# Kernel optimization log

Measured on AMD Instinct MI355X. Metric: run time of the kernel, lower is better.

## Reference

```python
import jax, jax.numpy as jnp
import numpy as np

IOU_HI = 0.5
IOU_LO = 0.0
ROI_BS = 256
POS_RATIO = 0.25
BG = 20  # background class id; valid classes 0..BG-1
NUM_POS = int(ROI_BS * POS_RATIO)
DELTAS_SCALING = np.array([10.0, 10.0, 5.0, 5.0], dtype=np.float32)  # (x, y, w, h)


def _make_boxes(key, shape):
    ka, kb = jax.random.split(key)
    c = jax.random.uniform(ka, shape + (2,), minval=0.05, maxval=0.95)
    s = jax.random.uniform(kb, shape + (2,), minval=0.02, maxval=0.4)
    lo = jnp.clip(c - s / 2, 0.0, 1.0)
    hi = jnp.clip(c + s / 2, 0.0, 1.0)
    return jnp.concatenate([lo, hi], -1)  # (y1, x1, y2, x2), normalized


def setup_inputs() -> dict:
    key = jax.random.key(0)
    k1, k2, k3 = jax.random.split(key, 3)
    B, N, G = 32, 12000, 200
    rois = _make_boxes(k1, (B, N))
    gt_boxes = _make_boxes(k2, (B, G))
    # class == BG marks a padded / invalid GT box
    gt_class_ids = jax.random.randint(k3, (B, G), 0, BG + 1).astype(jnp.int32)
    return {"rois": rois, "gt_class_ids": gt_class_ids, "gt_boxes": gt_boxes}


def _iou(rois, gts):
    # rois [N,4], gts [G,4] in (y1,x1,y2,x2) -> [N,G]
    y1 = jnp.maximum(rois[:, None, 0], gts[None, :, 0])
    x1 = jnp.maximum(rois[:, None, 1], gts[None, :, 1])
    y2 = jnp.minimum(rois[:, None, 2], gts[None, :, 2])
    x2 = jnp.minimum(rois[:, None, 3], gts[None, :, 3])
    inter = jnp.clip(y2 - y1, 0.0) * jnp.clip(x2 - x1, 0.0)
    ar = (rois[:, 2] - rois[:, 0]) * (rois[:, 3] - rois[:, 1])
    ag = (gts[:, 2] - gts[:, 0]) * (gts[:, 3] - gts[:, 1])
    return inter / (ar[:, None] + ag[None, :] - inter + 1e-8)


def _encode(r, g):
    # (tx, ty, tw, th) * scaling, r/g: [K,4] in (y1,x1,y2,x2)
    eps = 1e-6
    rh = r[:, 2] - r[:, 0]; rw = r[:, 3] - r[:, 1]
    rcy = r[:, 0] + rh / 2; rcx = r[:, 1] + rw / 2
    gh = g[:, 2] - g[:, 0]; gw = g[:, 3] - g[:, 1]
    gcy = g[:, 0] + gh / 2; gcx = g[:, 1] + gw / 2
    tx = (gcx - rcx) / (rw + eps)
    ty = (gcy - rcy) / (rh + eps)
    tw = jnp.log(jnp.maximum(gw, eps) / (rw + eps))
    th = jnp.log(jnp.maximum(gh, eps) / (rh + eps))
    return jnp.stack([tx, ty, tw, th], -1) * jnp.asarray(DELTAS_SCALING)


def _per_image(rois, gt_cls, gt_boxes):
    iou = _iou(rois, gt_boxes)                       # [N,G]
    valid_gt = gt_cls < BG
    iou = jnp.where(valid_gt[None, :], iou, -1.0)
    max_iou = iou.max(1)                             # [N]
    best_gt = iou.argmax(1)                          # [N]
    pos = max_iou >= IOU_HI
    neg = (max_iou < IOU_HI) & (max_iou >= IOU_LO)

    # deterministic sampling: highest-IoU positives / negatives first
    pos_val, pos_idx = jax.lax.top_k(jnp.where(pos, max_iou, -1.0), NUM_POS)
    pos_ok = pos_val > 0.0
    neg_val, neg_idx = jax.lax.top_k(jnp.where(neg, max_iou + 2.0, -1.0), ROI_BS)
    neg_ok = neg_val > 0.0

    rP = jnp.arange(NUM_POS, dtype=jnp.float32)
    rN = jnp.arange(ROI_BS, dtype=jnp.float32)
    prio = jnp.concatenate([jnp.where(pos_ok, 1e9 - rP, -1e9 - rP),
                            jnp.where(neg_ok, 1e6 - rN, -1e6 - rN)])
    cand_idx = jnp.concatenate([pos_idx, neg_idx])
    cand_pos = jnp.concatenate([pos_ok, jnp.zeros(ROI_BS, bool)])
    _, sel = jax.lax.top_k(prio, ROI_BS)
    sel_roi = cand_idx[sel]                          # [ROI_BS]
    sel_is_pos = cand_pos[sel]                       # [ROI_BS]

    labels = jnp.where(sel_is_pos, gt_cls[best_gt[sel_roi]], BG)
    rois_sel = rois[sel_roi]                         # [ROI_BS,4]
    gts_sel = gt_boxes[best_gt[sel_roi]]             # [ROI_BS,4]
    t = _encode(rois_sel, gts_sel) * sel_is_pos[:, None].astype(rois.dtype)

    cls_onehot = jax.nn.one_hot(labels, BG + 1, dtype=rois.dtype)   # [ROI_BS,BG+1]
    onehot_fg = jax.nn.one_hot(labels, BG, dtype=rois.dtype)        # zero row for bg
    mask4 = jnp.repeat(onehot_fg, 4, axis=1)                        # [ROI_BS,4*BG]
    deltas_full = (onehot_fg[:, :, None] * t[:, None, :]).reshape(ROI_BS, 4 * BG)
    reg = jnp.concatenate([mask4, deltas_full], -1)                 # [ROI_BS,8*BG]
    return rois_sel, cls_onehot, reg


def reference(rois, gt_class_ids, gt_boxes):
    return jax.vmap(_per_image)(rois, gt_class_ids, gt_boxes)
```

## Files before the change

### kernel.cpp

```cpp
#include <hip/hip_runtime.h>
#include <stdint.h>

#pragma clang fp contract(off)

#define BATCH 32
#define NROI  12000
#define NGT   200
#define BGCLS 20
#define ROIBS 256
#define NPOS  64
#define NBIN  1024
#define CAP   2048
#define TSEL  1024
#define VPT2  12
#define HSH   16
#define HST   (NBIN + 2)
#define DELTA 1e-6f

__device__ __forceinline__ void roi_maxiou_all(const float4* cbox, const float* carea,
                                               int nv, float ry1, float rx1,
                                               float ry2, float rx2,
                                               float& best, int& bj) {
#pragma clang fp contract(off)
  float ar = (ry2 - ry1) * (rx2 - rx1);
  best = -1.0f; bj = 0;
#pragma unroll 4
  for (int j = 0; j < nv; ++j) {
    float4 q = cbox[j];
    float yy1 = fmaxf(ry1, q.x);
    float xx1 = fmaxf(rx1, q.y);
    float yy2 = fminf(ry2, q.z);
    float xx2 = fminf(rx2, q.w);
    float inter = fmaxf(yy2 - yy1, 0.0f) * fmaxf(xx2 - xx1, 0.0f);
    float den = ((ar + carea[j]) - inter) + 1e-8f;
    float iou = inter / den;
    if (iou > best) { best = iou; bj = j; }
  }
}

__device__ __forceinline__ float approx_max(const float4* cbox, const float* carea,
                                            int nv, float4 r) {
  float ar = (r.z - r.x) * (r.w - r.y);
  float va = -1.0f, vb = -1.0f;
#pragma unroll 4
  for (int j = 0; j < nv; ++j) {
    float4 q = cbox[j];
    float yy1 = fmaxf(r.x, q.x);
    float xx1 = fmaxf(r.y, q.y);
    float yy2 = fminf(r.z, q.z);
    float xx2 = fminf(r.w, q.w);
    float inter = fmaxf(yy2 - yy1, 0.0f) * fmaxf(xx2 - xx1, 0.0f);
    float den = ((ar + carea[j]) - inter) + 1e-8f;
    float a = inter * __builtin_amdgcn_rcpf(den);
    if (j & 1) vb = fmaxf(vb, a); else va = fmaxf(va, a);
  }
  return fmaxf(va, vb);
}

__global__ __launch_bounds__(256) void k_ioumax(const float* __restrict__ rois,
                                                const int* __restrict__ gtc,
                                                const float* __restrict__ gtb,
                                                float* __restrict__ max_iou) {
  __shared__ float4 cbox[NGT];
  __shared__ float carea[NGT];
  __shared__ int snv, wtmp[4];
  const int b = blockIdx.y;
  const int tid = threadIdx.x;

  {
    bool valid = false; float4 p = make_float4(0.f, 0.f, 0.f, 0.f);
    if (tid < NGT) {
      p = *(const float4*)(gtb + ((size_t)b * NGT + tid) * 4);
      valid = gtc[(size_t)b * NGT + tid] < BGCLS;
    }
    unsigned long long m = __ballot(valid);
    int w = tid >> 6;
    if ((tid & 63) == 0) wtmp[w] = __popcll(m);
    __syncthreads();
    if (tid == 0) snv = wtmp[0] + wtmp[1] + wtmp[2] + wtmp[3];
    if (valid) {
      int off = 0;
      for (int i = 0; i < w; ++i) off += wtmp[i];
      int pos = off + __popcll(m & ((1ull << (tid & 63)) - 1ull));
      cbox[pos] = p;
      carea[pos] = (p.z - p.x) * (p.w - p.y);
    }
    __syncthreads();
  }
  int n = blockIdx.x * 256 + tid;
  if (n >= NROI) return;
  const float4 r = *(const float4*)(rois + ((size_t)b * NROI + n) * 4);
  max_iou[(size_t)b * NROI + n] = approx_max(cbox, carea, snv, r);
}

template <bool USE_WS>
__global__ __launch_bounds__(TSEL) void k_sel(const float* __restrict__ rois,
                                              const int* __restrict__ gtc,
                                              const float* __restrict__ gtb,
                                              const float* __restrict__ max_iou,
                                              float* __restrict__ out) {
#pragma clang fp contract(off)
  __shared__ float4 cbox[NGT];
  __shared__ float carea[NGT];
  __shared__ int ccls[NGT];
  __shared__ int snv, wtmp[16];
  __shared__ int wtot[16], wnext[16];
  __shared__ int plist[CAP];
  __shared__ unsigned long long keyl[CAP];
  __shared__ int bjl[CAP];
  __shared__ int hs[HSH][HST];
  __shared__ int ss[NBIN];
  __shared__ int sel_r[ROIBS];
  __shared__ int sel_b[ROIBS];
  __shared__ int scnt, sX, sT, sPos;
  const int b = blockIdx.x;
  const int tid = threadIdx.x;
  const int lane = tid & 63;

  {
    bool valid = false; float4 p = make_float4(0.f, 0.f, 0.f, 0.f); int cls = BGCLS;
    if (tid < NGT) {
      p = *(const float4*)(gtb + ((size_t)b * NGT + tid) * 4);
      cls = gtc[(size_t)b * NGT + tid];
      valid = (cls < BGCLS);
    }
    unsigned long long m = __ballot(valid);
    int w = tid >> 6;
    if ((tid & 63) == 0) wtmp[w] = __popcll(m);
    if (tid < ROIBS) { sel_r[tid] = 0; sel_b[tid] = 0; }
    __syncthreads();
    if (tid == 0) { int s = 0; for (int i = 0; i < 16; ++i) s += wtmp[i]; snv = s; }
    if (valid) {
      int off = 0;
      for (int i = 0; i < w; ++i) off += wtmp[i];
      int pos = off + __popcll(m & ((1ull << (tid & 63)) - 1ull));
      cbox[pos] = p;
      carea[pos] = (p.z - p.x) * (p.w - p.y);
      ccls[pos] = cls;
    }
    __syncthreads();
  }
  const int nv = snv;

  float v[VPT2];
#pragma unroll
  for (int i = 0; i < VPT2; ++i) {
    int n = tid + (i << 10);
    if (n < NROI) {
      if constexpr (USE_WS) {
        v[i] = max_iou[(size_t)b * NROI + n];
      } else {
        const float4 r = *(const float4*)(rois + ((size_t)b * NROI + n) * 4);
        v[i] = approx_max(cbox, carea, nv, r);
      }
    } else v[i] = -3.0f;
  }

  auto mkbin = [](unsigned kh, unsigned base, int shift) -> int {
    int bin = ((int)(kh - base)) >> shift;
    return max(min(bin, NBIN - 1), 0);
  };

  auto find_T = [&](int needv) -> int {
    if (tid == 0) sT = 0;
    __syncthreads();
    int cnt_bin = 0;
#pragma unroll
    for (int i = 0; i < HSH; ++i) cnt_bin += hs[i][tid];
    const int w = tid >> 6;
    int sfx = cnt_bin;
#pragma unroll
    for (int off = 1; off < 64; off <<= 1) {
      int t = __shfl_down(sfx, off, 64);
      sfx += (lane + off < 64) ? t : 0;
    }
    if (lane == 0) wtot[w] = sfx;
    __syncthreads();
    if (tid < 16) {
      int s = 0;
      for (int i = tid + 1; i < 16; ++i) s += wtot[i];
      wnext[tid] = s;
    }
    __syncthreads();
    const int suffix = sfx + wnext[w];
    ss[tid] = suffix;
    __syncthreads();
    int nxt = (tid + 1 < NBIN) ? ss[tid + 1] : 0;
    if (suffix >= needv && nxt < needv) sT = tid;
    __syncthreads();
    return sT;
  };

  auto rank_of = [&](unsigned long long ki, int cnt) -> int {
    int r0 = 0, r1 = 0, r2 = 0, r3 = 0;
    int j = 0;
    for (; j + 4 <= cnt; j += 4) {
      r0 += (keyl[j + 0] > ki);
      r1 += (keyl[j + 1] > ki);
      r2 += (keyl[j + 2] > ki);
      r3 += (keyl[j + 3] > ki);
    }
    for (; j < cnt; ++j) r0 += (keyl[j] > ki);
    return r0 + r1 + r2 + r3;
  };

  const int sh = tid & (HSH - 1);

  for (int i = tid; i < HSH * HST; i += TSEL) ((int*)hs)[i] = 0;
  if (tid == 0) { scnt = 0; sX = 0; sPos = 0; }
  __syncthreads();
#pragma unroll
  for (int i = 0; i < VPT2; ++i) {
    int n = tid + (i << 10);
    float x = v[i];
    bool inb = (n < NROI) && (x >= 0.5f - DELTA);
    if (inb) atomicAdd(&hs[sh][mkbin(__float_as_uint(x), 0x3F000000u, 13)], 1);
    bool bnd = inb && (x < 0.5f + DELTA);
    unsigned long long mx = __ballot(bnd);
    if (lane == 0 && mx) atomicAdd(&sX, __popcll(mx));
  }
  __syncthreads();
  const int XB = sX;
  const int Tp = max(find_T(NPOS + XB) - 2, 0);
#pragma unroll
  for (int i = 0; i < VPT2; ++i) {
    int n = tid + (i << 10);
    float x = v[i];
    bool pred = (n < NROI) && (x >= 0.5f - DELTA) &&
                (mkbin(__float_as_uint(x), 0x3F000000u, 13) >= Tp);
    unsigned long long mk = __ballot(pred);
    int c = __popcll(mk);
    int bs = 0;
    if (lane == 0 && c) bs = atomicAdd(&scnt, c);
    bs = __shfl(bs, 0, 64);
    if (pred) {
      int idx = bs + __popcll(mk & ((1ull << lane) - 1ull));
      if (idx < CAP) plist[idx] = n;
    }
  }
  __syncthreads();
  const int cntp = min(scnt, CAP);
  for (int i = tid; i < cntp; i += TSEL) {
    int n = plist[i];
    const float4 r = *(const float4*)(rois + ((size_t)b * NROI + n) * 4);
    float best; int bj;
    roi_maxiou_all(cbox, carea, nv, r.x, r.y, r.z, r.w, best, bj);
    bool ok = (best >= 0.5f);
    keyl[i] = ok ? (((unsigned long long)__float_as_uint(best) << 32)
                   | (unsigned)(0x7fffffff - n)) : 0ull;
    bjl[i] = bj;
    if (ok) atomicAdd(&sPos, 1);
  }
  __syncthreads();
  const int P = min(sPos, NPOS);
  for (int i = tid; i < cntp; i += TSEL) {
    unsigned long long ki = keyl[i];
    if (ki) {
      int rank = rank_of(ki, cntp);
      if (rank < P) {
        sel_r[rank] = 0x7fffffff - (int)(ki & 0xffffffffu);
        sel_b[rank] = bjl[i];
      }
    }
  }
  __syncthreads();

  const int need = ROIBS - P;
  for (int i = tid; i < HSH * HST; i += TSEL) ((int*)hs)[i] = 0;
  if (tid == 0) scnt = 0;
  __syncthreads();
#pragma unroll
  for (int i = 0; i < VPT2; ++i) {
    int n = tid + (i << 10);
    float x = v[i];
    if (n < NROI && x < 0.5f + DELTA)
      atomicAdd(&hs[sh][mkbin(__float_as_uint(x + 2.0f), 0x40000000u, 11)], 1);
  }
  __syncthreads();
  const int Tn = max(find_T(need + XB) - 2, 0);
#pragma unroll
  for (int i = 0; i < VPT2; ++i) {
    int n = tid + (i << 10);
    float x = v[i];
    bool pred = (n < NROI) && (x < 0.5f + DELTA) &&
                (mkbin(__float_as_uint(x + 2.0f), 0x40000000u, 11) >= Tn);
    unsigned long long mk = __ballot(pred);
    int c = __popcll(mk);
    int bs = 0;
    if (lane == 0 && c) bs = atomicAdd(&scnt, c);
    bs = __shfl(bs, 0, 64);
    if (pred) {
      int idx = bs + __popcll(mk & ((1ull << lane) - 1ull));
      if (idx < CAP) plist[idx] = n;
    }
  }
  __syncthreads();
  const int cntn = min(scnt, CAP);
  for (int i = tid; i < cntn; i += TSEL) {
    int n = plist[i];
    const float4 r = *(const float4*)(rois + ((size_t)b * NROI + n) * 4);
    float best; int bj;
    roi_maxiou_all(cbox, carea, nv, r.x, r.y, r.z, r.w, best, bj);
    bool ok = (best < 0.5f);
    keyl[i] = ok ? (((unsigned long long)__float_as_uint(best + 2.0f) << 32)
                   | (unsigned)(0x7fffffff - n)) : 0ull;
    bjl[i] = bj;
  }
  __syncthreads();
  for (int i = tid; i < cntn; i += TSEL) {
    unsigned long long ki = keyl[i];
    if (ki) {
      int rank = rank_of(ki, cntn);
      if (rank < need) {
        sel_r[P + rank] = 0x7fffffff - (int)(ki & 0xffffffffu);
        sel_b[P + rank] = bjl[i];
      }
    }
  }
  __syncthreads();

  {
    const int slot = tid >> 2, q = tid & 3;
    const int r = sel_r[slot];
    const int bj = sel_b[slot];
    const int isp = (slot < P) ? 1 : 0;
    const float4 rv = *(const float4*)(rois + ((size_t)b * NROI + r) * 4);
    float ry1 = rv.x, rx1 = rv.y, ry2 = rv.z, rx2 = rv.w;
    int label = isp ? ccls[bj] : BGCLS;

    float* out1 = out;
    float* out2 = out + (size_t)BATCH * ROIBS * 4;
    float* out3 = out + (size_t)BATCH * ROIBS * 25;
    size_t row = (size_t)b * ROIBS + slot;

    if (q == 0) {
      *(float4*)(out1 + row * 4) = rv;
      float* o2 = out2 + row * 21;
      for (int c = 0; c <= BGCLS; ++c) o2[c] = (c == label) ? 1.0f : 0.0f;
    }

    float t0 = 0.f, t1 = 0.f, t2 = 0.f, t3 = 0.f;
    if (isp) {
      const float eps = 1e-6f;
      float4 g = cbox[bj];
      float gy1 = g.x, gx1 = g.y, gy2 = g.z, gx2 = g.w;
      float rh = ry2 - ry1, rw = rx2 - rx1;
      float rcy = ry1 + rh * 0.5f, rcx = rx1 + rw * 0.5f;
      float gh = gy2 - gy1, gw = gx2 - gx1;
      float gcy = gy1 + gh * 0.5f, gcx = gx1 + gw * 0.5f;
      t0 = ((gcx - rcx) / (rw + eps)) * 10.0f;
      t1 = ((gcy - rcy) / (rh + eps)) * 10.0f;
      t2 = logf(fmaxf(gw, eps) / (rw + eps)) * 5.0f;
      t3 = logf(fmaxf(gh, eps) / (rh + eps)) * 5.0f;
    }
    int m0 = label * 4;
    float* o3 = out3 + row * 160;
    for (int c = q * 10; c < q * 10 + 10; ++c) {
      float4 wv = make_float4(0.f, 0.f, 0.f, 0.f);
      if (isp) {
        float* wp = &wv.x;
#pragma unroll
        for (int jj = 0; jj < 4; ++jj) {
          int e = c * 4 + jj;
          float x = 0.f;
          if (e >= m0 && e < m0 + 4) x = 1.0f;
          int d = e - 80 - m0;
          if (d == 0) x = t0; else if (d == 1) x = t1;
          else if (d == 2) x = t2; else if (d == 3) x = t3;
          wp[jj] = x;
        }
      }
      *(float4*)(o3 + c * 4) = wv;
    }
  }
}

extern "C" void kernel_launch(void* const* d_in, const int* in_sizes, int n_in,
                              void* d_out, int out_size, void* d_ws, size_t ws_size,
                              hipStream_t stream) {
  const float* rois = (const float*)d_in[0];
  const int*   gtc  = (const int*)d_in[1];
  const float* gtb  = (const float*)d_in[2];
  float*       out  = (float*)d_out;

  size_t need = (size_t)BATCH * NROI * sizeof(float);
  if (d_ws && ws_size >= need) {
    float* mi = (float*)d_ws;
    k_ioumax<<<dim3((NROI + 255) / 256, BATCH), 256, 0, stream>>>(rois, gtc, gtb, mi);
    k_sel<true><<<BATCH, TSEL, 0, stream>>>(rois, gtc, gtb, mi, out);
  } else {
    k_sel<false><<<BATCH, TSEL, 0, stream>>>(rois, gtc, gtb, nullptr, out);
  }
}
```

Before: 98.68 us.

## Split per-image selection into parallel positive/negative blocks plus emit kernel

Measured after the change: 86.34 us. -12.5%, faster.

```diff
diff --git a/kernel.cpp b/kernel.cpp
--- a/kernel.cpp
+++ b/kernel.cpp
@@ -57,6 +57,38 @@
   return fmaxf(va, vb);
 }
 
+template <int NTHR>
+__device__ __forceinline__ int stage_gt(float4* cbox, float* carea, int* ccls,
+                                        int* snv, int* wtmp,
+                                        const float* gtb, const int* gtc, int b) {
+  const int tid = threadIdx.x;
+  bool valid = false; float4 p = make_float4(0.f, 0.f, 0.f, 0.f); int cls = BGCLS;
+  if (tid < NGT) {
+    p = *(const float4*)(gtb + ((size_t)b * NGT + tid) * 4);
+    cls = gtc[(size_t)b * NGT + tid];
+    valid = (cls < BGCLS);
+  }
+  unsigned long long m = __ballot(valid);
+  int w = tid >> 6;
+  if ((tid & 63) == 0) wtmp[w] = __popcll(m);
+  __syncthreads();
+  if (tid == 0) {
+    int s = 0;
+    for (int i = 0; i < NTHR / 64; ++i) s += wtmp[i];
+    *snv = s;
+  }
+  if (valid) {
+    int off = 0;
+    for (int i = 0; i < w; ++i) off += wtmp[i];
+    int pos = off + __popcll(m & ((1ull << (tid & 63)) - 1ull));
+    cbox[pos] = p;
+    carea[pos] = (p.z - p.x) * (p.w - p.y);
+    if (ccls) ccls[pos] = cls;
+  }
+  __syncthreads();
+  return *snv;
+}
+
 __global__ __launch_bounds__(256) void k_ioumax(const float* __restrict__ rois,
                                                 const int* __restrict__ gtc,
                                                 const float* __restrict__ gtb,
@@ -65,40 +97,253 @@
   __shared__ float carea[NGT];
   __shared__ int snv, wtmp[4];
   const int b = blockIdx.y;
-  const int tid = threadIdx.x;
-
-  {
-    bool valid = false; float4 p = make_float4(0.f, 0.f, 0.f, 0.f);
-    if (tid < NGT) {
-      p = *(const float4*)(gtb + ((size_t)b * NGT + tid) * 4);
-      valid = gtc[(size_t)b * NGT + tid] < BGCLS;
-    }
-    unsigned long long m = __ballot(valid);
-    int w = tid >> 6;
-    if ((tid & 63) == 0) wtmp[w] = __popcll(m);
-    __syncthreads();
-    if (tid == 0) snv = wtmp[0] + wtmp[1] + wtmp[2] + wtmp[3];
-    if (valid) {
-      int off = 0;
-      for (int i = 0; i < w; ++i) off += wtmp[i];
-      int pos = off + __popcll(m & ((1ull << (tid & 63)) - 1ull));
-      cbox[pos] = p;
-      carea[pos] = (p.z - p.x) * (p.w - p.y);
-    }
-    __syncthreads();
-  }
-  int n = blockIdx.x * 256 + tid;
+  const int nv = stage_gt<256>(cbox, carea, nullptr, &snv, wtmp, gtb, gtc, b);
+  int n = blockIdx.x * 256 + threadIdx.x;
   if (n >= NROI) return;
   const float4 r = *(const float4*)(rois + ((size_t)b * NROI + n) * 4);
-  max_iou[(size_t)b * NROI + n] = approx_max(cbox, carea, snv, r);
-}
-
-template <bool USE_WS>
-__global__ __launch_bounds__(TSEL) void k_sel(const float* __restrict__ rois,
-                                              const int* __restrict__ gtc,
-                                              const float* __restrict__ gtb,
-                                              const float* __restrict__ max_iou,
-                                              float* __restrict__ out) {
+  max_iou[(size_t)b * NROI + n] = approx_max(cbox, carea, nv, r);
+}
+
+__global__ __launch_bounds__(TSEL) void k_selA(const float* __restrict__ rois,
+                                               const int* __restrict__ gtc,
+                                               const float* __restrict__ gtb,
+                                               const float* __restrict__ mi,
+                                               int* __restrict__ posCnt,
+                                               int* __restrict__ posN,
+                                               int* __restrict__ posBJ,
+                                               int* __restrict__ negCnt,
+                                               int* __restrict__ negN,
+                                               int* __restrict__ negBJ) {
+#pragma clang fp contract(off)
+  __shared__ float4 cbox[NGT];
+  __shared__ float carea[NGT];
+  __shared__ int snv, wtmp[16];
+  __shared__ int wtot[16], wnext[16];
+  __shared__ int plist[CAP];
+  __shared__ unsigned long long keyl[CAP];
+  __shared__ int bjl[CAP];
+  __shared__ int hs[HSH][HST];
+  __shared__ int ss[NBIN];
+  __shared__ int scnt, sX, sT, sOk;
+  const int b = blockIdx.x >> 1;
+  const bool isPos = (blockIdx.x & 1) == 0;
+  const int tid = threadIdx.x;
+  const int lane = tid & 63;
+  const int nv = stage_gt<TSEL>(cbox, carea, nullptr, &snv, wtmp, gtb, gtc, b);
+
+  float v[VPT2];
+#pragma unroll
+  for (int i = 0; i < VPT2; ++i) {
+    int n = tid + (i << 10);
+    v[i] = (n < NROI) ? mi[(size_t)b * NROI + n] : -3.0f;
+  }
+
+  auto mkbin = [](unsigned kh, unsigned base, int shift) -> int {
+    int bin = ((int)(kh - base)) >> shift;
+    return max(min(bin, NBIN - 1), 0);
+  };
+  const unsigned base = isPos ? 0x3F000000u : 0x40000000u;
+  const int shift = isPos ? 13 : 11;
+
+  for (int i = tid; i < HSH * HST; i += TSEL) ((int*)hs)[i] = 0;
+  if (tid == 0) { scnt = 0; sX = 0; sOk = 0; }
+  __syncthreads();
+  const int sh = tid & (HSH - 1);
+#pragma unroll
+  for (int i = 0; i < VPT2; ++i) {
+    int n = tid + (i << 10);
+    float x = v[i];
+    bool inb = isPos ? ((n < NROI) && (x >= 0.5f - DELTA))
+                     : ((n < NROI) && (x < 0.5f + DELTA));
+    if (inb) {
+      unsigned kh = __float_as_uint(isPos ? x : (x + 2.0f));
+      atomicAdd(&hs[sh][mkbin(kh, base, shift)], 1);
+    }
+    bool bnd = (n < NROI) && (x >= 0.5f - DELTA) && (x < 0.5f + DELTA);
+    unsigned long long mx = __ballot(bnd);
+    if (lane == 0 && mx) atomicAdd(&sX, __popcll(mx));
+  }
+  __syncthreads();
+  const int limitWant = isPos ? NPOS : ROIBS;
+  const int needv = limitWant + sX;
+
+  {
+    if (tid == 0) sT = 0;
+    __syncthreads();
+    int cnt_bin = 0;
+#pragma unroll
+    for (int i = 0; i < HSH; ++i) cnt_bin += hs[i][tid];
+    const int w = tid >> 6;
+    int sfx = cnt_bin;
+#pragma unroll
+    for (int off = 1; off < 64; off <<= 1) {
+      int t = __shfl_down(sfx, off, 64);
+      sfx += (lane + off < 64) ? t : 0;
+    }
+    if (lane == 0) wtot[w] = sfx;
+    __syncthreads();
+    if (tid < 16) {
+      int s = 0;
+      for (int i = tid + 1; i < 16; ++i) s += wtot[i];
+      wnext[tid] = s;
+    }
+    __syncthreads();
+    const int suffix = sfx + wnext[w];
+    ss[tid] = suffix;
+    __syncthreads();
+    int nxt = (tid + 1 < NBIN) ? ss[tid + 1] : 0;
+    if (suffix >= needv && nxt < needv) sT = tid;
+    __syncthreads();
+  }
+  const int Tc = max(sT - 2, 0);
+
+#pragma unroll
+  for (int i = 0; i < VPT2; ++i) {
+    int n = tid + (i << 10);
+    float x = v[i];
+    bool inb = isPos ? ((n < NROI) && (x >= 0.5f - DELTA))
+                     : ((n < NROI) && (x < 0.5f + DELTA));
+    bool pred = inb &&
+        (mkbin(__float_as_uint(isPos ? x : (x + 2.0f)), base, shift) >= Tc);
+    unsigned long long mk = __ballot(pred);
+    int c = __popcll(mk);
+    int bs = 0;
+    if (lane == 0 && c) bs = atomicAdd(&scnt, c);
+    bs = __shfl(bs, 0, 64);
+    if (pred) {
+      int idx = bs + __popcll(mk & ((1ull << lane) - 1ull));
+      if (idx < CAP) plist[idx] = n;
+    }
+  }
+  __syncthreads();
+  const int cnt = min(scnt, CAP);
+
+  for (int i = tid; i < cnt; i += TSEL) {
+    int n = plist[i];
+    const float4 r = *(const float4*)(rois + ((size_t)b * NROI + n) * 4);
+    float best; int bj;
+    roi_maxiou_all(cbox, carea, nv, r.x, r.y, r.z, r.w, best, bj);
+    bool ok = isPos ? (best >= 0.5f) : (best < 0.5f);
+    unsigned kh = __float_as_uint(isPos ? best : (best + 2.0f));
+    keyl[i] = ok ? (((unsigned long long)kh << 32) | (unsigned)(0x7fffffff - n))
+                 : 0ull;
+    bjl[i] = bj;
+    if (ok) atomicAdd(&sOk, 1);
+  }
+  __syncthreads();
+  const int limit = min(sOk, limitWant);
+  if (tid == 0) { if (isPos) posCnt[b] = limit; else negCnt[b] = limit; }
+
+  int* dstN = isPos ? (posN + (size_t)b * NPOS) : (negN + (size_t)b * ROIBS);
+  int* dstB = isPos ? (posBJ + (size_t)b * NPOS) : (negBJ + (size_t)b * ROIBS);
+  for (int i = tid; i < cnt; i += TSEL) {
+    unsigned long long ki = keyl[i];
+    if (ki) {
+      int r0 = 0, r1 = 0, r2 = 0, r3 = 0;
+      int j = 0;
+      for (; j + 4 <= cnt; j += 4) {
+        r0 += (keyl[j + 0] > ki);
+        r1 += (keyl[j + 1] > ki);
+        r2 += (keyl[j + 2] > ki);
+        r3 += (keyl[j + 3] > ki);
+      }
+      for (; j < cnt; ++j) r0 += (keyl[j] > ki);
+      int rank = r0 + r1 + r2 + r3;
+      if (rank < limit) {
+        dstN[rank] = 0x7fffffff - (int)(ki & 0xffffffffu);
+        dstB[rank] = bjl[i];
+      }
+    }
+  }
+}
+
+__global__ __launch_bounds__(TSEL) void k_emit(const float* __restrict__ rois,
+                                               const int* __restrict__ gtc,
+                                               const float* __restrict__ gtb,
+                                               const int* __restrict__ posCnt,
+                                               const int* __restrict__ posN,
+                                               const int* __restrict__ posBJ,
+                                               const int* __restrict__ negCnt,
+                                               const int* __restrict__ negN,
+                                               const int* __restrict__ negBJ,
+                                               float* __restrict__ out) {
+#pragma clang fp contract(off)
+  __shared__ float4 cbox[NGT];
+  __shared__ float carea[NGT];
+  __shared__ int ccls[NGT];
+  __shared__ int snv, wtmp[16];
+  const int b = blockIdx.x;
+  const int tid = threadIdx.x;
+  stage_gt<TSEL>(cbox, carea, ccls, &snv, wtmp, gtb, gtc, b);
+
+  const int P = min(posCnt[b], NPOS);
+  const int NC = negCnt[b];
+  const int slot = tid >> 2, q = tid & 3;
+  int r = 0, bj = 0, isp = 0;
+  if (slot < P) {
+    r = posN[(size_t)b * NPOS + slot];
+    bj = posBJ[(size_t)b * NPOS + slot];
+    isp = 1;
+  } else {
+    int j = slot - P;
+    if (j < NC) {
+      r = negN[(size_t)b * ROIBS + j];
+      bj = negBJ[(size_t)b * ROIBS + j];
+    }
+  }
+  const float4 rv = *(const float4*)(rois + ((size_t)b * NROI + r) * 4);
+  float ry1 = rv.x, rx1 = rv.y, ry2 = rv.z, rx2 = rv.w;
+  int label = isp ? ccls[bj] : BGCLS;
+
+  float* out1 = out;
+  float* out2 = out + (size_t)BATCH * ROIBS * 4;
+  float* out3 = out + (size_t)BATCH * ROIBS * 25;
+  size_t row = (size_t)b * ROIBS + slot;
+
+  if (q == 0) {
+    *(float4*)(out1 + row * 4) = rv;
+    float* o2 = out2 + row * 21;
+    for (int c = 0; c <= BGCLS; ++c) o2[c] = (c == label) ? 1.0f : 0.0f;
+  }
+
+  float t0 = 0.f, t1 = 0.f, t2 = 0.f, t3 = 0.f;
+  if (isp) {
+    const float eps = 1e-6f;
+    float4 g = cbox[bj];
+    float rh = ry2 - ry1, rw = rx2 - rx1;
+    float rcy = ry1 + rh * 0.5f, rcx = rx1 + rw * 0.5f;
+    float gh = g.z - g.x, gw = g.w - g.y;
+    float gcy = g.x + gh * 0.5f, gcx = g.y + gw * 0.5f;
+    t0 = ((gcx - rcx) / (rw + eps)) * 10.0f;
+    t1 = ((gcy - rcy) / (rh + eps)) * 10.0f;
+    t2 = logf(fmaxf(gw, eps) / (rw + eps)) * 5.0f;
+    t3 = logf(fmaxf(gh, eps) / (rh + eps)) * 5.0f;
+  }
+  int m0 = label * 4;
+  float* o3 = out3 + row * 160;
+  for (int c = q * 10; c < q * 10 + 10; ++c) {
+    float4 wv = make_float4(0.f, 0.f, 0.f, 0.f);
+    if (isp) {
+      float* wp = &wv.x;
+#pragma unroll
+      for (int jj = 0; jj < 4; ++jj) {
+        int e = c * 4 + jj;
+        float x = 0.f;
+        if (e >= m0 && e < m0 + 4) x = 1.0f;
+        int d = e - 80 - m0;
+        if (d == 0) x = t0; else if (d == 1) x = t1;
+        else if (d == 2) x = t2; else if (d == 3) x = t3;
+        wp[jj] = x;
+      }
+    }
+    *(float4*)(o3 + c * 4) = wv;
+  }
+}
+
+__global__ __launch_bounds__(TSEL) void k_sel_mono(const float* __restrict__ rois,
+                                                   const int* __restrict__ gtc,
+                                                   const float* __restrict__ gtb,
+                                                   float* __restrict__ out) {
 #pragma clang fp contract(off)
   __shared__ float4 cbox[NGT];
   __shared__ float carea[NGT];
@@ -116,43 +361,16 @@
   const int b = blockIdx.x;
   const int tid = threadIdx.x;
   const int lane = tid & 63;
-
-  {
-    bool valid = false; float4 p = make_float4(0.f, 0.f, 0.f, 0.f); int cls = BGCLS;
-    if (tid < NGT) {
-      p = *(const float4*)(gtb + ((size_t)b * NGT + tid) * 4);
-      cls = gtc[(size_t)b * NGT + tid];
-      valid = (cls < BGCLS);
-    }
-    unsigned long long m = __ballot(valid);
-    int w = tid >> 6;
-    if ((tid & 63) == 0) wtmp[w] = __popcll(m);
-    if (tid < ROIBS) { sel_r[tid] = 0; sel_b[tid] = 0; }
-    __syncthreads();
-    if (tid == 0) { int s = 0; for (int i = 0; i < 16; ++i) s += wtmp[i]; snv = s; }
-    if (valid) {
-      int off = 0;
-      for (int i = 0; i < w; ++i) off += wtmp[i];
-      int pos = off + __popcll(m & ((1ull << (tid & 63)) - 1ull));
-      cbox[pos] = p;
-      carea[pos] = (p.z - p.x) * (p.w - p.y);
-      ccls[pos] = cls;
-    }
-    __syncthreads();
-  }
-  const int nv = snv;
+  if (tid < ROIBS) { sel_r[tid] = 0; sel_b[tid] = 0; }
+  const int nv = stage_gt<TSEL>(cbox, carea, ccls, &snv, wtmp, gtb, gtc, b);
 
   float v[VPT2];
 #pragma unroll
   for (int i = 0; i < VPT2; ++i) {
     int n = tid + (i << 10);
     if (n < NROI) {
-      if constexpr (USE_WS) {
-        v[i] = max_iou[(size_t)b * NROI + n];
-      } else {
-        const float4 r = *(const float4*)(rois + ((size_t)b * NROI + n) * 4);
-        v[i] = approx_max(cbox, carea, nv, r);
-      }
+      const float4 r = *(const float4*)(rois + ((size_t)b * NROI + n) * 4);
+      v[i] = approx_max(cbox, carea, nv, r);
     } else v[i] = -3.0f;
   }
 
@@ -160,7 +378,6 @@
     int bin = ((int)(kh - base)) >> shift;
     return max(min(bin, NBIN - 1), 0);
   };
-
   auto find_T = [&](int needv) -> int {
     if (tid == 0) sT = 0;
     __syncthreads();
@@ -190,7 +407,6 @@
     __syncthreads();
     return sT;
   };
-
   auto rank_of = [&](unsigned long long ki, int cnt) -> int {
     int r0 = 0, r1 = 0, r2 = 0, r3 = 0;
     int j = 0;
@@ -203,7 +419,6 @@
     for (; j < cnt; ++j) r0 += (keyl[j] > ki);
     return r0 + r1 + r2 + r3;
   };
-
   const int sh = tid & (HSH - 1);
 
   for (int i = tid; i < HSH * HST; i += TSEL) ((int*)hs)[i] = 0;
@@ -327,27 +542,23 @@
     const float4 rv = *(const float4*)(rois + ((size_t)b * NROI + r) * 4);
     float ry1 = rv.x, rx1 = rv.y, ry2 = rv.z, rx2 = rv.w;
     int label = isp ? ccls[bj] : BGCLS;
-
     float* out1 = out;
     float* out2 = out + (size_t)BATCH * ROIBS * 4;
     float* out3 = out + (size_t)BATCH * ROIBS * 25;
     size_t row = (size_t)b * ROIBS + slot;
-
     if (q == 0) {
       *(float4*)(out1 + row * 4) = rv;
       float* o2 = out2 + row * 21;
       for (int c = 0; c <= BGCLS; ++c) o2[c] = (c == label) ? 1.0f : 0.0f;
     }
-
     float t0 = 0.f, t1 = 0.f, t2 = 0.f, t3 = 0.f;
     if (isp) {
       const float eps = 1e-6f;
       float4 g = cbox[bj];
-      float gy1 = g.x, gx1 = g.y, gy2 = g.z, gx2 = g.w;
       float rh = ry2 - ry1, rw = rx2 - rx1;
       float rcy = ry1 + rh * 0.5f, rcx = rx1 + rw * 0.5f;
-      float gh = gy2 - gy1, gw = gx2 - gx1;
-      float gcy = gy1 + gh * 0.5f, gcx = gx1 + gw * 0.5f;
+      float gh = g.z - g.x, gw = g.w - g.y;
+      float gcy = g.x + gh * 0.5f, gcx = g.y + gw * 0.5f;
       t0 = ((gcx - rcx) / (rw + eps)) * 10.0f;
       t1 = ((gcy - rcy) / (rh + eps)) * 10.0f;
       t2 = logf(fmaxf(gw, eps) / (rw + eps)) * 5.0f;
@@ -383,12 +594,25 @@
   const float* gtb  = (const float*)d_in[2];
   float*       out  = (float*)d_out;
 
-  size_t need = (size_t)BATCH * NROI * sizeof(float);
+  const size_t A = (size_t)BATCH * NROI;
+  const size_t nint = 32 + (size_t)BATCH * NPOS * 2 + 32 + (size_t)BATCH * ROIBS * 2;
+  const size_t need = (A + nint) * 4;
   if (d_ws && ws_size >= need) {
     float* mi = (float*)d_ws;
+    int* p = (int*)((float*)d_ws + A);
+    int* posCnt = p;             p += 32;
+    int* posN   = p;             p += BATCH * NPOS;
+    int* posBJ  = p;             p += BATCH * NPOS;
+    int* negCnt = p;             p += 32;
+    int* negN   = p;             p += BATCH * ROIBS;
+    int* negBJ  = p;
     k_ioumax<<<dim3((NROI + 255) / 256, BATCH), 256, 0, stream>>>(rois, gtc, gtb, mi);
-    k_sel<true><<<BATCH, TSEL, 0, stream>>>(rois, gtc, gtb, mi, out);
+    k_selA<<<BATCH * 2, TSEL, 0, stream>>>(rois, gtc, gtb, mi,
+                                           posCnt, posN, posBJ,
+                                           negCnt, negN, negBJ);
+    k_emit<<<BATCH, TSEL, 0, stream>>>(rois, gtc, gtb, posCnt, posN, posBJ,
+                                       negCnt, negN, negBJ, out);
   } else {
-    k_sel<false><<<BATCH, TSEL, 0, stream>>>(rois, gtc, gtb, nullptr, out);
-  }
-}
+    k_sel_mono<<<BATCH, TSEL, 0, stream>>>(rois, gtc, gtb, out);
+  }
+}
```
